# Optimization experiments

Measured on AMD Instinct MI355X. Metric: run time of the kernel, lower is better.

Reference implementation:

```python
import jax, jax.numpy as jnp
import numpy as np

DECAY = 0.99
EPS_VQ = 1e-5
EPS_LN = 1e-5


def setup_inputs() -> dict:
    key = jax.random.key(0)
    ks = jax.random.split(key, 6)
    N, DIN, D, K = 32768, 1024, 512, 1024
    return {
        "x": jax.random.normal(ks[0], (N, DIN), dtype=jnp.float32),
        "enc_w": jax.random.normal(ks[1], (DIN, D), dtype=jnp.float32) * (1.0 / np.sqrt(DIN)),
        "enc_b": jnp.zeros((D,), jnp.float32),
        "ln_g": jnp.ones((D,), jnp.float32),
        "ln_b": jnp.zeros((D,), jnp.float32),
        "dec_w": jax.random.normal(ks[2], (D, DIN), dtype=jnp.float32) * (1.0 / np.sqrt(D)),
        "dec_b": jnp.zeros((DIN,), jnp.float32),
        "embeddings": jax.random.normal(ks[3], (K, D), dtype=jnp.float32),
        "cluster_size": jnp.ones((K,), jnp.float32),
        "ema_embed_sum": jax.random.normal(ks[4], (K, D), dtype=jnp.float32),
    }


def _layernorm(h, g, b):
    mu = jnp.mean(h, axis=-1, keepdims=True)
    var = jnp.var(h, axis=-1, keepdims=True)
    return (h - mu) * jax.lax.rsqrt(var + EPS_LN) * g + b


def reference(x, enc_w, enc_b, ln_g, ln_b, dec_w, dec_b, embeddings, cluster_size, ema_embed_sum):
    K = embeddings.shape[0]
    # encoder: Linear + LayerNorm
    z_e = _layernorm(x @ enc_w + enc_b, ln_g, ln_b)  # [N, D]
    # pairwise squared L2 distances, expanded GEMM form (same argmin as (z-e)^2.sum)
    d = (jnp.sum(z_e * z_e, axis=1, keepdims=True)
         - 2.0 * (z_e @ embeddings.T)
         + jnp.sum(embeddings * embeddings, axis=1)[None, :])  # [N, K]
    indices = jnp.argmin(d, axis=1)  # [N]
    z_q = embeddings[indices]  # gather [N, D]
    # EMA codebook update (training path; buffers, no grad)
    zd = jax.lax.stop_gradient(z_e)
    counts = jax.ops.segment_sum(jnp.ones_like(indices, jnp.float32), indices, num_segments=K)
    embed_sum = jax.ops.segment_sum(zd, indices, num_segments=K)  # one_hot.T @ z
    new_cluster_size = DECAY * cluster_size + (1.0 - DECAY) * counts
    new_ema_embed_sum = DECAY * ema_embed_sum + (1.0 - DECAY) * embed_sum
    n = jnp.sum(new_cluster_size)
    cs = (new_cluster_size + EPS_VQ) / (n + K * EPS_VQ) * n
    new_embeddings = new_ema_embed_sum / cs[:, None]
    # commitment loss + straight-through estimator
    commit_loss = jnp.mean((z_e - jax.lax.stop_gradient(z_q)) ** 2)
    z_q_st = z_e + jax.lax.stop_gradient(z_q - z_e)
    x_recon = z_q_st @ dec_w + dec_b
    return (x_recon, commit_loss, indices, z_e, z_q_st,
            new_embeddings, new_cluster_size, new_ema_embed_sum)
```

## Files before the change

kernel.cpp:

```cpp
#include <hip/hip_runtime.h>

typedef unsigned long long u64;
typedef unsigned int u32;
typedef _Float16 f16;
typedef _Float16 f16x8 __attribute__((ext_vector_type(8)));
typedef float f32x4 __attribute__((ext_vector_type(4)));

#define MFMA16(a, b, c) __builtin_amdgcn_mfma_f32_16x16x32_f16(a, b, c, 0, 0, 0)

#define NROWS 32768
#define DIN   1024
#define DM    512
#define KC    1024
#define SPLIT_SC  1024.0f
#define SPLIT_INV 0.0009765625f
#define CHSZ  32
#define MAXCH 2048
#define MARGIN 0.5f

#define OFF_XR   0ull
#define OFF_CL   33554432ull
#define OFF_IDX  33554433ull
#define OFF_ZE   33587201ull
#define OFF_ZQ   50364417ull
#define OFF_NE   67141633ull
#define OFF_NCS  67665921ull
#define OFF_NEMA 67666945ull

#define WS_ZNORM   2359296ull
#define WS_IDX     2490368ull
#define WS_COUNTS  2621440ull
#define WS_STARTS  2625536ull
#define WS_OFFW    2629632ull
#define WS_ROWLIST 2633728ull
#define WS_CSD     2764800ull
#define WS_ENORM   2769920ull
#define WS2_CAND   (4ull<<20)
#define WS2_WT1    (36ull<<20)
#define WS2_WT2    (37ull<<20)
#define WS2_DT     (38ull<<20)
#define WS2_E1     (39ull<<20)
#define WS3_CHPFX  (41ull<<20)
#define WS3_CHCODE ((41ull<<20) + 8192)
#define WS3_CPART  ((41ull<<20) + 16384)
#define WS3_PART   ((41ull<<20) + 65536)

__device__ inline void gload16(const f16* g, f16* l) {
  __builtin_amdgcn_global_load_lds((const __attribute__((address_space(1))) void*)g,
                                   (__attribute__((address_space(3))) void*)l, 16, 0, 0);
}

__device__ inline f16x8 ldfrag32(const f16* p, int row, int kc) {
  return *(const f16x8*)(p + row * 32 + ((kc ^ ((row >> 1) & 3)) << 3));
}

__device__ inline void stage32(const f16* gbase, int ld, int row0, int k0,
                               f16* lds, int t) {
  int r = t >> 2, c = t & 3;
  int cs = c ^ ((r >> 1) & 3);
  gload16(gbase + (size_t)(row0 + r) * ld + k0 + cs * 8, lds + t * 8);
}

__device__ inline void stageA256(const f16* gbase, int ld, int row0, int k0,
                                 f16* lds, int t) {
#pragma unroll
  for (int h = 0; h < 2; h++) {
    int e = t + h * 512;
    int r = e >> 2, c = e & 3;
    int cs = c ^ ((r >> 1) & 3);
    gload16(gbase + (size_t)(row0 + r) * ld + k0 + cs * 8, lds + e * 8);
  }
}

#define BAR2      { asm volatile("s_waitcnt lgkmcnt(0)" ::: "memory"); \
                    __builtin_amdgcn_s_barrier(); \
                    asm volatile("" ::: "memory"); }

__device__ inline u32 enc_score(float s) {
  u32 kb = __float_as_uint(s);
  return (kb & 0x80000000u) ? ~kb : (kb | 0x80000000u);
}
__device__ inline float dec_score(u32 u) {
  u32 b = (u & 0x80000000u) ? (u & 0x7fffffffu) : ~u;
  return __uint_as_float(b);
}

__global__ __launch_bounds__(256) void k_prep(const float* __restrict__ enc_w,
                                              const float* __restrict__ dec_w,
                                              const float* __restrict__ emb,
                                              f16* __restrict__ wt1,
                                              f16* __restrict__ wt2,
                                              f16* __restrict__ dT,
                                              f16* __restrict__ e1,
                                              float* __restrict__ enorm,
                                              int* __restrict__ counts) {
  __shared__ float tile[32][33];
  int bid = blockIdx.x, t = threadIdx.x;
  if (bid < 1024) {
    const float* W;
    f16 *o1, *o2;
    int K, N, bx, by;
    if (bid < 512) {
      W = enc_w; o1 = wt1; o2 = wt2; K = DIN; N = DM;
      bx = bid & 15; by = bid >> 4;
    } else {
      int b2 = bid - 512;
      W = dec_w; o1 = dT; o2 = nullptr; K = DM; N = DIN;
      bx = b2 & 31; by = b2 >> 5;
    }
    int tx = t & 31, ty = t >> 5;
    int nb = bx * 32, kb = by * 32;
#pragma unroll
    for (int i = 0; i < 32; i += 8)
      tile[ty + i][tx] = W[(size_t)(kb + ty + i) * N + nb + tx];
    __syncthreads();
#pragma unroll
    for (int i = 0; i < 32; i += 8) {
      float v = tile[tx][ty + i];
      f16 h = (f16)v;
      size_t o = (size_t)(nb + ty + i) * K + kb + tx;
      o1[o] = h;
      if (o2) o2[o] = (f16)((v - (float)h) * SPLIT_SC);
    }
  } else if (bid < 1536) {
    int tid = (bid - 1024) * 256 + t;
    for (int i = tid; i < KC * DM; i += 131072) e1[i] = (f16)emb[i];
  } else if (bid < 1792) {
    int k = (bid - 1536) * 4 + (t >> 6), lane = t & 63;
    float s = 0.f;
#pragma unroll
    for (int j = 0; j < 8; j++) {
      float v = emb[(size_t)k * DM + lane + j * 64];
      s = fmaf(v, v, s);
    }
#pragma unroll
    for (int m = 1; m < 64; m <<= 1) s += __shfl_xor(s, m, 64);
    if (lane == 0) enorm[k] = s;
  } else {
    int i = (bid - 1792) * 256 + t;
    if (i < KC) counts[i] = 0;
  }
}

__global__ __launch_bounds__(512) void k_genc4(const float* __restrict__ x,
                                               const f16* __restrict__ wt1,
                                               const f16* __restrict__ wt2,
                                               const float* __restrict__ bias,
                                               float* __restrict__ dst) {
  __shared__ __align__(16) f16 A1[128 * 32], A2[128 * 32];
  __shared__ __align__(16) f16 B1[2][128 * 32], B2[2][128 * 32];
  int t = threadIdx.x, lane = t & 63, wid = t >> 6;
  int wm = wid >> 2, wn = wid & 3;
  int l = blockIdx.x;
  int xcd = l & 7, s = l >> 3, ct = s & 3;
  int p = ((s >> 2) << 3) | xcd;
  int m0 = p * 128, n0 = ct * 128;
  int r = t >> 2, cg = t & 3;
  int cslot = cg ^ ((r >> 1) & 3);
  const float* ax = x + (size_t)(m0 + r) * DIN + cg * 8;
  f32x4 accA[4][2] = {}, accB[4][2] = {};

#define GCONV(v0, v1)                                                       \
  {                                                                         \
    float a_[8] = {v0.x, v0.y, v0.z, v0.w, v1.x, v1.y, v1.z, v1.w};         \
    f16 h1_[8], h2_[8];                                                     \
    _Pragma("unroll") for (int j_ = 0; j_ < 8; j_++) {                      \
      f16 h_ = (f16)a_[j_];                                                 \
      h1_[j_] = h_;                                                         \
      h2_[j_] = (f16)((a_[j_] - (float)h_) * SPLIT_SC);                     \
    }                                                                       \
    *(f16x8*)(A1 + r * 32 + cslot * 8) = *(f16x8*)h1_;                      \
    *(f16x8*)(A2 + r * 32 + cslot * 8) = *(f16x8*)h2_;                      \
  }

#define GCOMP(buf)                                                          \
  {                                                                         \
    int kc_ = lane >> 4;                                                    \
    f16x8 a1f[4], a2f[4], b1f[2], b2f[2];                                   \
    _Pragma("unroll") for (int m_ = 0; m_ < 4; m_++) {                      \
      int row_ = wm * 64 + m_ * 16 + (lane & 15);                           \
      a1f[m_] = ldfrag32(A1, row_, kc_);                                    \
      a2f[m_] = ldfrag32(A2, row_, kc_);                                    \
    }                                                                       \
    _Pragma("unroll") for (int n_ = 0; n_ < 2; n_++) {                      \
      int row_ = wn * 32 + n_ * 16 + (lane & 15);                           \
      b1f[n_] = ldfrag32(B1[buf], row_, kc_);                               \
      b2f[n_] = ldfrag32(B2[buf], row_, kc_);                               \
    }                                                                       \
    _Pragma("unroll") for (int m_ = 0; m_ < 4; m_++)                        \
      _Pragma("unroll") for (int n_ = 0; n_ < 2; n_++) {                    \
        accA[m_][n_] = MFMA16(a1f[m_], b1f[n_], accA[m_][n_]);              \
        accB[m_][n_] = MFMA16(a1f[m_], b2f[n_], accB[m_][n_]);              \
        accB[m_][n_] = MFMA16(a2f[m_], b1f[n_], accB[m_][n_]);              \
      }                                                                     \
  }

  float4 c0 = *(const float4*)(ax);
  float4 c1 = *(const float4*)(ax + 4);
  float4 n0v = *(const float4*)(ax + 32);
  float4 n1v = *(const float4*)(ax + 36);
  stage32(wt1, DIN, n0, 0, B1[0], t);
  stage32(wt2, DIN, n0, 0, B2[0], t);
  asm volatile("s_waitcnt vmcnt(4)" ::: "memory");

  for (int it = 0; it < 32; ++it) {
    GCONV(c0, c1);
    if (it + 1 < 32) {
      stage32(wt1, DIN, n0, (it + 1) * 32, B1[(it + 1) & 1], t);
      stage32(wt2, DIN, n0, (it + 1) * 32, B2[(it + 1) & 1], t);
    }
    float4 f0, f1;
    if (it + 2 < 32) {
      f0 = *(const float4*)(ax + (it + 2) * 32);
      f1 = *(const float4*)(ax + (it + 2) * 32 + 4);
    }
    if (it <= 29) {
      asm volatile("s_waitcnt vmcnt(4) lgkmcnt(0)" ::: "memory");
    } else if (it == 30) {
      asm volatile("s_waitcnt vmcnt(2) lgkmcnt(0)" ::: "memory");
    } else {
      asm volatile("s_waitcnt vmcnt(0) lgkmcnt(0)" ::: "memory");
    }
    __builtin_amdgcn_sched_barrier(0);
    __builtin_amdgcn_s_barrier();
    asm volatile("" ::: "memory");
    GCOMP(it & 1);
    BAR2;
    c0 = n0v; c1 = n1v; n0v = f0; n1v = f1;
  }
#undef GCONV
#undef GCOMP

#pragma unroll
  for (int m = 0; m < 4; m++)
#pragma unroll
    for (int n = 0; n < 2; n++)
#pragma unroll
      for (int j = 0; j < 4; j++) {
        int row = m0 + wm * 64 + m * 16 + (lane >> 4) * 4 + j;
        int col = n0 + wn * 32 + n * 16 + (lane & 15);
        dst[(size_t)row * DM + col] = accA[m][n][j] + SPLIT_INV * accB[m][n][j] + bias[col];
      }
}

__global__ __launch_bounds__(512, 4) void k_dist4(const f16* __restrict__ z1,
                                                  const f16* __restrict__ e1,
                                                  const float* __restrict__ enorm,
                                                  u64* __restrict__ cand) {
  __shared__ __align__(16) f16 A[3][256 * 32];
  __shared__ __align__(16) f16 B[3][128 * 32];
  int t = threadIdx.x, lane = t & 63, wid = t >> 6;
  int wr = wid >> 1, wc = wid & 1;
  int l = blockIdx.x;
  int xcd = l & 7, s = l >> 3, ct = s & 7;
  int p = ((s >> 3) << 3) | xcd;
  int r0 = p * 256, c0 = ct * 128;
  f32x4 acc[4][4] = {};
  int kc = lane >> 4;

  stageA256(z1, DM, r0, 0, A[0], t);
  stage32(e1, DM, c0, 0, B[0], t);

  for (int it = 0; it < 16; ++it) {
    int buf = it % 3;
    if (it < 15) {
      int nb = (it + 1) % 3;
      int k0n = (it + 1) * 32;
      stageA256(z1, DM, r0, k0n, A[nb], t);
      stage32(e1, DM, c0, k0n, B[nb], t);
      asm volatile("s_waitcnt vmcnt(3)" ::: "memory");
    } else {
      asm volatile("s_waitcnt vmcnt(0)" ::: "memory");
    }
    __builtin_amdgcn_sched_barrier(0);
    __builtin_amdgcn_s_barrier();
    asm volatile("" ::: "memory");
    f16x8 af[4], bf[4];
#pragma unroll
    for (int m = 0; m < 4; m++)
      af[m] = ldfrag32(A[buf], wr * 64 + m * 16 + (lane & 15), kc);
#pragma unroll
    for (int n = 0; n < 4; n++)
      bf[n] = ldfrag32(B[buf], wc * 64 + n * 16 + (lane & 15), kc);
#pragma unroll
    for (int m = 0; m < 4; m++)
#pragma unroll
      for (int n = 0; n < 4; n++) acc[m][n] = MFMA16(af[m], bf[n], acc[m][n]);
  }

  __syncthreads();
  u64 (*cand_s)[4] = (u64 (*)[4])(&A[0][0]);
  float en[4];
#pragma unroll
  for (int n = 0; n < 4; n++)
    en[n] = enorm[c0 + wc * 64 + n * 16 + (lane & 15)];
#pragma unroll
  for (int m = 0; m < 4; m++)
#pragma unroll
    for (int j = 0; j < 4; j++) {
      int r_l = wr * 64 + m * 16 + (lane >> 4) * 4 + j;
      u64 lo = ~0ull, hi = ~0ull;
#pragma unroll
      for (int n = 0; n < 4; n++) {
        int col = c0 + wc * 64 + n * 16 + (lane & 15);
        float sc = fmaf(-2.0f, acc[m][n][j], en[n]);
        u64 k = ((u64)enc_score(sc) << 32) | (u32)col;
        if (k < lo) { hi = lo; lo = k; }
        else if (k < hi) { hi = k; }
      }
#pragma unroll
      for (int msk = 1; msk < 16; msk <<= 1) {
        u64 lo2 = __shfl_xor(lo, msk, 64);
        u64 hi2 = __shfl_xor(hi, msk, 64);
        u64 nlo = lo < lo2 ? lo : lo2;
        u64 losr = lo < lo2 ? lo2 : lo;
        u64 nh = hi < hi2 ? hi : hi2;
        hi = losr < nh ? losr : nh;
        lo = nlo;
      }
      if ((lane & 15) == 0) {
        cand_s[r_l][wc * 2] = lo;
        cand_s[r_l][wc * 2 + 1] = hi;
      }
    }
  __syncthreads();
  if (t < 256) {
    u64 b0 = ~0ull, b1 = ~0ull;
#pragma unroll
    for (int i = 0; i < 4; i++) {
      u64 k = cand_s[t][i];
      if (k < b0) { b1 = b0; b0 = k; }
      else if (k < b1) { b1 = k; }
    }
    u64* dst = cand + ((size_t)(r0 + t) * 16 + ct * 2);
    dst[0] = b0;
    dst[1] = b1;
  }
}

__global__ __launch_bounds__(512) void k_edgemm(const f16* __restrict__ e1,
                                                const f16* __restrict__ dT,
                                                const float* __restrict__ bias,
                                                float* __restrict__ ED) {
  __shared__ __align__(16) f16 A[3][128 * 32], B[3][128 * 32];
  int t = threadIdx.x, lane = t & 63, wid = t >> 6;
  int wm = wid >> 2, wn = wid & 3;
  int r0 = (blockIdx.x >> 3) * 128, c0 = (blockIdx.x & 7) * 128;
  f32x4 acc[4][2] = {};
  int kc = lane >> 4;

  stage32(e1, DM, r0, 0, A[0], t);
  stage32(dT, DM, c0, 0, B[0], t);

  for (int it = 0; it < 16; ++it) {
    int buf = it % 3;
    if (it < 15) {
      int nb = (it + 1) % 3;
      int k0n = (it + 1) * 32;
      stage32(e1, DM, r0, k0n, A[nb], t);
      stage32(dT, DM, c0, k0n, B[nb], t);
      asm volatile("s_waitcnt vmcnt(2)" ::: "memory");
    } else {
      asm volatile("s_waitcnt vmcnt(0)" ::: "memory");
    }
    __builtin_amdgcn_sched_barrier(0);
    __builtin_amdgcn_s_barrier();
    asm volatile("" ::: "memory");
    f16x8 af[4], bf[2];
#pragma unroll
    for (int m = 0; m < 4; m++)
      af[m] = ldfrag32(A[buf], wm * 64 + m * 16 + (lane & 15), kc);
#pragma unroll
    for (int n = 0; n < 2; n++)
      bf[n] = ldfrag32(B[buf], wn * 32 + n * 16 + (lane & 15), kc);
#pragma unroll
    for (int m = 0; m < 4; m++)
#pragma unroll
      for (int n = 0; n < 2; n++) acc[m][n] = MFMA16(af[m], bf[n], acc[m][n]);
  }

#pragma unroll
  for (int m = 0; m < 4; m++)
#pragma unroll
    for (int n = 0; n < 2; n++)
#pragma unroll
      for (int j = 0; j < 4; j++) {
        int row = r0 + wm * 64 + m * 16 + (lane >> 4) * 4 + j;
        int col = c0 + wn * 32 + n * 16 + (lane & 15);
        ED[(size_t)row * DIN + col] = acc[m][n][j] + bias[col];
      }
}

__global__ __launch_bounds__(256) void k_gatherx(const int* __restrict__ idxws,
                                                 const float* __restrict__ ED,
                                                 float* __restrict__ xr) {
  int t = threadIdx.x, r0 = blockIdx.x * 16;
  __shared__ int idx_s[16];
  if (t < 16) idx_s[t] = idxws[r0 + t];
  __syncthreads();
  for (int rr = 0; rr < 16; rr++) {
    int R = r0 + rr;
    const float4* src = (const float4*)(ED + (size_t)idx_s[rr] * DIN);
    float4* dst = (float4*)(xr + (size_t)R * DIN);
    dst[t] = src[t];
  }
}

__global__ __launch_bounds__(256) void k_resolve(const u64* __restrict__ cand,
                                                 const float* __restrict__ znorm,
                                                 const float* __restrict__ enorm,
                                                 const float* __restrict__ emb,
                                                 float* __restrict__ out,
                                                 int* __restrict__ idxws,
                                                 int* __restrict__ counts,
                                                 float* __restrict__ cpart) {
  int t = threadIdx.x, bid = blockIdx.x;
  int r0 = bid * 16;
  __shared__ u64 key_s[256];
  __shared__ int idx_s[16];
  __shared__ float commit_s[16];
  __shared__ int flagcnt_s;
  __shared__ int flagrow_s[16];
  key_s[t] = cand[(size_t)r0 * 16 + t];
  if (t == 0) flagcnt_s = 0;
  __syncthreads();

  if (t < 16) {
    u64 best = ~0ull;
#pragma unroll
    for (int i = 0; i < 16; i++) {
      u64 k = key_s[t * 16 + i];
      best = k < best ? k : best;
    }
    float smin = dec_score((u32)(best >> 32));
    float thr = smin + MARGIN;
    int nc = 0;
#pragma unroll
    for (int i = 0; i < 16; i++)
      if (dec_score((u32)(key_s[t * 16 + i] >> 32)) <= thr) nc++;
    idx_s[t] = (int)(u32)(best & 0xffffffffull);
    commit_s[t] = znorm[r0 + t] + smin;
    if (nc > 1) {
      int pz = atomicAdd(&flagcnt_s, 1);
      flagrow_s[pz] = t;
    }
  }
  __syncthreads();

  if (t < 64) {
    int nf = flagcnt_s;
    for (int fi = 0; fi < nf; fi++) {
      int lr = flagrow_s[fi];
      int R = r0 + lr;
      u64 amin = ~0ull;
      for (int i = 0; i < 16; i++) {
        u64 k = key_s[lr * 16 + i];
        amin = k < amin ? k : amin;
      }
      float thr = dec_score((u32)(amin >> 32)) + MARGIN;
      float zn = znorm[R];
      const float* z = out + OFF_ZE + (size_t)R * DM;
      u64 bestk = ~0ull;
      for (int i = 0; i < 16; i++) {
        u64 k = key_s[lr * 16 + i];
        if (dec_score((u32)(k >> 32)) > thr) continue;
        int c = (int)(u32)(k & 0xffffffffull);
        const float* e = emb + (size_t)c * DM;
        float pdot = 0.f;
#pragma unroll
        for (int j = 0; j < 8; j++) pdot = fmaf(z[t + j * 64], e[t + j * 64], pdot);
#pragma unroll
        for (int m = 1; m < 64; m <<= 1) pdot += __shfl_xor(pdot, m, 64);
        float d = fmaf(-2.0f, pdot, zn) + enorm[c];
        u64 pk = ((u64)enc_score(d) << 32) | (u32)c;
        bestk = pk < bestk ? pk : bestk;
      }
      if (t == 0) {
        idx_s[lr] = (int)(u32)(bestk & 0xffffffffull);
        commit_s[lr] = dec_score((u32)(bestk >> 32));
      }
    }
  }
  __syncthreads();

  if (t < 16) {
    int R = r0 + t;
    int idx = idx_s[t];
    out[OFF_IDX + R] = (float)idx;
    idxws[R] = idx;
    atomicAdd(counts + idx, 1);
  }
  __syncthreads();
  for (int rr = 0; rr < 16; rr++) {
    int R = r0 + rr;
    const float* e = emb + (size_t)idx_s[rr] * DM;
    float* zq = out + OFF_ZQ + (size_t)R * DM;
#pragma unroll
    for (int j = 0; j < 2; j++) {
      int c = t + j * 256;
      zq[c] = e[c];
    }
  }
  if (t == 0) {
    float s = 0.f;
#pragma unroll
    for (int i = 0; i < 16; i++) s += commit_s[i];
    cpart[bid] = s;
  }
}

__global__ __launch_bounds__(256) void k_ln3(float* __restrict__ ze,
                                             const float* __restrict__ g,
                                             const float* __restrict__ b,
                                             f16* __restrict__ z1,
                                             float* __restrict__ znorm) {
  int t = threadIdx.x, lane = t & 63, wid = t >> 6;
  int R = blockIdx.x * 4 + wid;
  float* row = ze + (size_t)R * DM;
  float v[8];
  float s = 0.f, sq = 0.f;
#pragma unroll
  for (int j = 0; j < 8; j++) {
    v[j] = row[lane + j * 64];
    s += v[j];
    sq = fmaf(v[j], v[j], sq);
  }
#pragma unroll
  for (int m = 1; m < 64; m <<= 1) {
    s += __shfl_xor(s, m, 64);
    sq += __shfl_xor(sq, m, 64);
  }
  float mu = s * (1.f / DM);
  float var = sq * (1.f / DM) - mu * mu;
  float rs = rsqrtf(var + 1e-5f);
  float zn = 0.f;
#pragma unroll
  for (int j = 0; j < 8; j++) {
    int c = lane + j * 64;
    float o = (v[j] - mu) * rs * g[c] + b[c];
    row[c] = o;
    z1[(size_t)R * DM + c] = (f16)o;
    zn = fmaf(o, o, zn);
  }
#pragma unroll
  for (int m = 1; m < 64; m <<= 1) zn += __shfl_xor(zn, m, 64);
  if (lane == 0) znorm[R] = zn;
}

__global__ __launch_bounds__(1024) void k_scan(const int* __restrict__ counts,
                                               const float* __restrict__ cs_in,
                                               float* __restrict__ out,
                                               int* __restrict__ starts,
                                               int* __restrict__ offw,
                                               float* __restrict__ csd,
                                               const float* __restrict__ cpart,
                                               int* __restrict__ chpfx,
                                               int* __restrict__ chcode) {
  __shared__ float f[1024];
  __shared__ int ib[1024];
  int t = threadIdx.x;
  f[t] = cpart[t] + cpart[t + 1024];
  __syncthreads();
  for (int s = 512; s > 0; s >>= 1) {
    if (t < s) f[t] += f[t + s];
    __syncthreads();
  }
  if (t == 0) out[OFF_CL] = f[0] * (1.f / ((float)NROWS * (float)DM));
  __syncthreads();

  int cnt = counts[t];
  float ncs = 0.99f * cs_in[t] + 0.01f * (float)cnt;
  out[OFF_NCS + t] = ncs;
  f[t] = ncs;
  __syncthreads();
  for (int s = 512; s > 0; s >>= 1) {
    if (t < s) f[t] += f[t + s];
    __syncthreads();
  }
  float n = f[0];
  csd[t] = (ncs + 1e-5f) / (n + (float)KC * 1e-5f) * n;
  ib[t] = cnt;
  __syncthreads();
  for (int s = 1; s < 1024; s <<= 1) {
    int y = (t >= s) ? ib[t - s] : 0;
    __syncthreads();
    ib[t] += y;
    __syncthreads();
  }
  int excl = ib[t] - cnt;
  starts[t] = excl;
  offw[t] = excl;
  int nch = (cnt + CHSZ - 1) / CHSZ;
  __syncthreads();
  ib[t] = nch;
  __syncthreads();
  for (int s = 1; s < 1024; s <<= 1) {
    int y = (t >= s) ? ib[t - s] : 0;
    __syncthreads();
    ib[t] += y;
    __syncthreads();
  }
  int chx = ib[t] - nch;
  chpfx[t] = chx;
  if (t == KC - 1) chpfx[KC] = ib[t];
  for (int j = 0; j < nch; j++) chcode[chx + j] = t;
}

__global__ __launch_bounds__(256) void k_scatter(const int* __restrict__ idxws,
                                                 int* __restrict__ offw,
                                                 int* __restrict__ rowlist) {
  int r = blockIdx.x * 256 + threadIdx.x;
  int idx = idxws[r];
  int pos = atomicAdd(offw + idx, 1);
  rowlist[pos] = r;
}

__global__ __launch_bounds__(128) void k_partsum(const int* __restrict__ chpfx,
                                                 const int* __restrict__ chcode,
                                                 const int* __restrict__ starts,
                                                 const int* __restrict__ counts,
                                                 const int* __restrict__ rowlist,
                                                 const float* __restrict__ out,
                                                 float* __restrict__ part) {
  int c = blockIdx.x, t = threadIdx.x;
  if (c >= chpfx[KC]) return;
  int code = chcode[c];
  int j = c - chpfx[code];
  int ofs = starts[code] + j * CHSZ;
  int len = min(CHSZ, counts[code] - j * CHSZ);
  __shared__ int rl[CHSZ];
  if (t < len) rl[t] = rowlist[ofs + t];
  __syncthreads();
  const float* zeb = out + OFF_ZE;
  float a0 = 0.f, a1 = 0.f, a2 = 0.f, a3 = 0.f;
  for (int i = 0; i < len; i++) {
    const float* z = zeb + (size_t)rl[i] * DM;
    a0 += z[t];
    a1 += z[t + 128];
    a2 += z[t + 256];
    a3 += z[t + 384];
  }
  float* pp = part + (size_t)c * DM;
  pp[t] = a0;
  pp[t + 128] = a1;
  pp[t + 256] = a2;
  pp[t + 384] = a3;
}

__global__ __launch_bounds__(128) void k_codesum2(const int* __restrict__ chpfx,
                                                  const float* __restrict__ part,
                                                  const float* __restrict__ ema_in,
                                                  const float* __restrict__ csd,
                                                  float* __restrict__ out) {
  int k = blockIdx.x, t = threadIdx.x;
  int base = chpfx[k], nch = chpfx[k + 1] - base;
  float a0 = 0.f, a1 = 0.f, a2 = 0.f, a3 = 0.f;
  for (int i = 0; i < nch; i++) {
    const float* pp = part + (size_t)(base + i) * DM;
    a0 += pp[t];
    a1 += pp[t + 128];
    a2 += pp[t + 256];
    a3 += pp[t + 384];
  }
  float cs = csd[k];
  float sum[4] = {a0, a1, a2, a3};
#pragma unroll
  for (int j = 0; j < 4; j++) {
    int c = t + j * 128;
    float e = 0.99f * ema_in[(size_t)k * DM + c] + 0.01f * sum[j];
    out[OFF_NEMA + (size_t)k * DM + c] = e;
    out[OFF_NE + (size_t)k * DM + c] = e / cs;
  }
}

extern "C" void kernel_launch(void* const* d_in, const int* in_sizes, int n_in,
                              void* d_out, int out_size, void* d_ws, size_t ws_size,
                              hipStream_t stream) {
  (void)in_sizes; (void)n_in; (void)out_size; (void)ws_size;
  const float* x = (const float*)d_in[0];
  const float* enc_w = (const float*)d_in[1];
  const float* enc_b = (const float*)d_in[2];
  const float* ln_g = (const float*)d_in[3];
  const float* ln_b = (const float*)d_in[4];
  const float* dec_w = (const float*)d_in[5];
  const float* dec_b = (const float*)d_in[6];
  const float* emb = (const float*)d_in[7];
  const float* cs_in = (const float*)d_in[8];
  const float* ema_in = (const float*)d_in[9];
  float* out = (float*)d_out;
  char* ws = (char*)d_ws;
  float* znorm = (float*)(ws + WS_ZNORM);
  int* idxws = (int*)(ws + WS_IDX);
  int* counts = (int*)(ws + WS_COUNTS);
  int* starts = (int*)(ws + WS_STARTS);
  int* offw = (int*)(ws + WS_OFFW);
  int* rowlist = (int*)(ws + WS_ROWLIST);
  float* csd = (float*)(ws + WS_CSD);
  float* enorm = (float*)(ws + WS_ENORM);
  u64* cand = (u64*)(ws + WS2_CAND);
  float* ED = (float*)(ws + WS2_CAND);
  f16* wt1 = (f16*)(ws + WS2_WT1);
  f16* wt2 = (f16*)(ws + WS2_WT2);
  f16* dT = (f16*)(ws + WS2_DT);
  f16* e1 = (f16*)(ws + WS2_E1);
  int* chpfx = (int*)(ws + WS3_CHPFX);
  int* chcode = (int*)(ws + WS3_CHCODE);
  float* cpart = (float*)(ws + WS3_CPART);
  float* part = (float*)(ws + WS3_PART);
  f16* z1 = (f16*)out;

  k_prep<<<dim3(1796), dim3(256), 0, stream>>>(enc_w, dec_w, emb, wt1, wt2, dT,
                                               e1, enorm, counts);
  k_genc4<<<dim3(1024), dim3(512), 0, stream>>>(x, wt1, wt2, enc_b, out + OFF_ZE);
  k_ln3<<<dim3(8192), dim3(256), 0, stream>>>(out + OFF_ZE, ln_g, ln_b, z1, znorm);
  k_dist4<<<dim3(1024), dim3(512), 0, stream>>>(z1, e1, enorm, cand);
  k_resolve<<<dim3(2048), dim3(256), 0, stream>>>(cand, znorm, enorm, emb, out,
                                                  idxws, counts, cpart);
  k_edgemm<<<dim3(64), dim3(512), 0, stream>>>(e1, dT, dec_b, ED);
  k_scan<<<dim3(1), dim3(1024), 0, stream>>>(counts, cs_in, out, starts, offw, csd,
                                             cpart, chpfx, chcode);
  k_scatter<<<dim3(NROWS / 256), dim3(256), 0, stream>>>(idxws, offw, rowlist);
  k_partsum<<<dim3(MAXCH), dim3(128), 0, stream>>>(chpfx, chcode, starts, counts,
                                                   rowlist, out, part);
  k_codesum2<<<dim3(KC), dim3(128), 0, stream>>>(chpfx, part, ema_in, csd, out);
  k_gatherx<<<dim3(2048), dim3(256), 0, stream>>>(idxws, ED, out + OFF_XR);
}
```

Before: 336.7 us.

## Use single fp16 encoder GEMM and recompute ambiguous rows in fp32

Replaces the split-precision (hi/lo fp16, three MFMAs per tile) encoder GEMM with a plain fp16 GEMM over a pre-converted fp16 copy of x, using a larger 256x128 tile with a triple-buffered LDS pipeline. Rows whose nearest-code decision falls within a margin are collected into a global flag list, and a new kernel recomputes their encoder output and LayerNorm in fp32 to re-pick the code and patch indices, counts and z_q. This cuts MFMA work and the on-the-fly conversion, at the cost of an extra x conversion pass and an fp32 fix-up pass. z_e, the commit loss and the EMA sums still come from the lower-precision GEMM, so output accuracy may drop.

```diff
diff --git a/kernel.cpp b/kernel.cpp
--- a/kernel.cpp
+++ b/kernel.cpp
@@ -4,6 +4,7 @@
 typedef unsigned int u32;
 typedef _Float16 f16;
 typedef _Float16 f16x8 __attribute__((ext_vector_type(8)));
+typedef _Float16 f16x4 __attribute__((ext_vector_type(4)));
 typedef float f32x4 __attribute__((ext_vector_type(4)));
 
 #define MFMA16(a, b, c) __builtin_amdgcn_mfma_f32_16x16x32_f16(a, b, c, 0, 0, 0)
@@ -13,10 +14,10 @@
 #define DM    512
 #define KC    1024
 #define SPLIT_SC  1024.0f
-#define SPLIT_INV 0.0009765625f
 #define CHSZ  32
 #define MAXCH 2048
 #define MARGIN 0.5f
+#define ZB    8
 
 #define OFF_XR   0ull
 #define OFF_CL   33554432ull
@@ -27,6 +28,7 @@
 #define OFF_NCS  67665921ull
 #define OFF_NEMA 67666945ull
 
+#define WS_FLAG    2097152ull
 #define WS_ZNORM   2359296ull
 #define WS_IDX     2490368ull
 #define WS_COUNTS  2621440ull
@@ -37,13 +39,14 @@
 #define WS_ENORM   2769920ull
 #define WS2_CAND   (4ull<<20)
 #define WS2_WT1    (36ull<<20)
-#define WS2_WT2    (37ull<<20)
 #define WS2_DT     (38ull<<20)
 #define WS2_E1     (39ull<<20)
 #define WS3_CHPFX  (41ull<<20)
 #define WS3_CHCODE ((41ull<<20) + 8192)
 #define WS3_CPART  ((41ull<<20) + 16384)
+#define WS3_NFLAG  ((41ull<<20) + 32768)
 #define WS3_PART   ((41ull<<20) + 65536)
+
 
 __device__ inline void gload16(const f16* g, f16* l) {
   __builtin_amdgcn_global_load_lds((const __attribute__((address_space(1))) void*)g,
@@ -72,10 +75,6 @@
   }
 }
 
-#define BAR2      { asm volatile("s_waitcnt lgkmcnt(0)" ::: "memory"); \
-                    __builtin_amdgcn_s_barrier(); \
-                    asm volatile("" ::: "memory"); }
-
 __device__ inline u32 enc_score(float s) {
   u32 kb = __float_as_uint(s);
   return (kb & 0x80000000u) ? ~kb : (kb | 0x80000000u);
@@ -88,24 +87,26 @@
 __global__ __launch_bounds__(256) void k_prep(const float* __restrict__ enc_w,
                                               const float* __restrict__ dec_w,
                                               const float* __restrict__ emb,
+                                              const float* __restrict__ x,
                                               f16* __restrict__ wt1,
-                                              f16* __restrict__ wt2,
                                               f16* __restrict__ dT,
                                               f16* __restrict__ e1,
+                                              f16* __restrict__ x16,
                                               float* __restrict__ enorm,
-                                              int* __restrict__ counts) {
+                                              int* __restrict__ counts,
+                                              int* __restrict__ nflag) {
   __shared__ float tile[32][33];
   int bid = blockIdx.x, t = threadIdx.x;
   if (bid < 1024) {
     const float* W;
-    f16 *o1, *o2;
+    f16* o1;
     int K, N, bx, by;
     if (bid < 512) {
-      W = enc_w; o1 = wt1; o2 = wt2; K = DIN; N = DM;
+      W = enc_w; o1 = wt1; K = DIN; N = DM;
       bx = bid & 15; by = bid >> 4;
     } else {
       int b2 = bid - 512;
-      W = dec_w; o1 = dT; o2 = nullptr; K = DM; N = DIN;
+      W = dec_w; o1 = dT; K = DM; N = DIN;
       bx = b2 & 31; by = b2 >> 5;
     }
     int tx = t & 31, ty = t >> 5;
@@ -115,13 +116,8 @@
       tile[ty + i][tx] = W[(size_t)(kb + ty + i) * N + nb + tx];
     __syncthreads();
 #pragma unroll
-    for (int i = 0; i < 32; i += 8) {
-      float v = tile[tx][ty + i];
-      f16 h = (f16)v;
-      size_t o = (size_t)(nb + ty + i) * K + kb + tx;
-      o1[o] = h;
-      if (o2) o2[o] = (f16)((v - (float)h) * SPLIT_SC);
-    }
+    for (int i = 0; i < 32; i += 8)
+      o1[(size_t)(nb + ty + i) * K + kb + tx] = (f16)tile[tx][ty + i];
   } else if (bid < 1536) {
     int tid = (bid - 1024) * 256 + t;
     for (int i = tid; i < KC * DM; i += 131072) e1[i] = (f16)emb[i];
@@ -136,110 +132,74 @@
 #pragma unroll
     for (int m = 1; m < 64; m <<= 1) s += __shfl_xor(s, m, 64);
     if (lane == 0) enorm[k] = s;
-  } else {
+  } else if (bid < 1796) {
     int i = (bid - 1792) * 256 + t;
     if (i < KC) counts[i] = 0;
-  }
-}
-
-__global__ __launch_bounds__(512) void k_genc4(const float* __restrict__ x,
-                                               const f16* __restrict__ wt1,
-                                               const f16* __restrict__ wt2,
-                                               const float* __restrict__ bias,
-                                               float* __restrict__ dst) {
-  __shared__ __align__(16) f16 A1[128 * 32], A2[128 * 32];
-  __shared__ __align__(16) f16 B1[2][128 * 32], B2[2][128 * 32];
+    if (bid == 1792 && t == 0) nflag[0] = 0;
+  } else {
+    size_t base = (size_t)(bid - 1796) * 16384;
+    for (int i = t; i < 4096; i += 256) {
+      float4 v = *(const float4*)(x + base + (size_t)i * 4);
+      f16 h4[4] = {(f16)v.x, (f16)v.y, (f16)v.z, (f16)v.w};
+      *(f16x4*)(x16 + base + (size_t)i * 4) = *(f16x4*)h4;
+    }
+  }
+}
+
+__global__ __launch_bounds__(512, 4) void k_genc1p(const f16* __restrict__ x16,
+                                                   const f16* __restrict__ wt1,
+                                                   const float* __restrict__ bias,
+                                                   float* __restrict__ dst) {
+  __shared__ __align__(16) f16 A[3][256 * 32];
+  __shared__ __align__(16) f16 B[3][128 * 32];
   int t = threadIdx.x, lane = t & 63, wid = t >> 6;
-  int wm = wid >> 2, wn = wid & 3;
+  int wr = wid >> 1, wc = wid & 1;
   int l = blockIdx.x;
   int xcd = l & 7, s = l >> 3, ct = s & 3;
   int p = ((s >> 2) << 3) | xcd;
-  int m0 = p * 128, n0 = ct * 128;
-  int r = t >> 2, cg = t & 3;
-  int cslot = cg ^ ((r >> 1) & 3);
-  const float* ax = x + (size_t)(m0 + r) * DIN + cg * 8;
-  f32x4 accA[4][2] = {}, accB[4][2] = {};
-
-#define GCONV(v0, v1)                                                       \
-  {                                                                         \
-    float a_[8] = {v0.x, v0.y, v0.z, v0.w, v1.x, v1.y, v1.z, v1.w};         \
-    f16 h1_[8], h2_[8];                                                     \
-    _Pragma("unroll") for (int j_ = 0; j_ < 8; j_++) {                      \
-      f16 h_ = (f16)a_[j_];                                                 \
-      h1_[j_] = h_;                                                         \
-      h2_[j_] = (f16)((a_[j_] - (float)h_) * SPLIT_SC);                     \
-    }                                                                       \
-    *(f16x8*)(A1 + r * 32 + cslot * 8) = *(f16x8*)h1_;                      \
-    *(f16x8*)(A2 + r * 32 + cslot * 8) = *(f16x8*)h2_;                      \
-  }
-
-#define GCOMP(buf)                                                          \
-  {                                                                         \
-    int kc_ = lane >> 4;                                                    \
-    f16x8 a1f[4], a2f[4], b1f[2], b2f[2];                                   \
-    _Pragma("unroll") for (int m_ = 0; m_ < 4; m_++) {                      \
-      int row_ = wm * 64 + m_ * 16 + (lane & 15);                           \
-      a1f[m_] = ldfrag32(A1, row_, kc_);                                    \
-      a2f[m_] = ldfrag32(A2, row_, kc_);                                    \
-    }                                                                       \
-    _Pragma("unroll") for (int n_ = 0; n_ < 2; n_++) {                      \
-      int row_ = wn * 32 + n_ * 16 + (lane & 15);                           \
-      b1f[n_] = ldfrag32(B1[buf], row_, kc_);                               \
-      b2f[n_] = ldfrag32(B2[buf], row_, kc_);                               \
-    }                                                                       \
-    _Pragma("unroll") for (int m_ = 0; m_ < 4; m_++)                        \
-      _Pragma("unroll") for (int n_ = 0; n_ < 2; n_++) {                    \
-        accA[m_][n_] = MFMA16(a1f[m_], b1f[n_], accA[m_][n_]);              \
-        accB[m_][n_] = MFMA16(a1f[m_], b2f[n_], accB[m_][n_]);              \
-        accB[m_][n_] = MFMA16(a2f[m_], b1f[n_], accB[m_][n_]);              \
-      }                                                                     \
-  }
-
-  float4 c0 = *(const float4*)(ax);
-  float4 c1 = *(const float4*)(ax + 4);
-  float4 n0v = *(const float4*)(ax + 32);
-  float4 n1v = *(const float4*)(ax + 36);
-  stage32(wt1, DIN, n0, 0, B1[0], t);
-  stage32(wt2, DIN, n0, 0, B2[0], t);
-  asm volatile("s_waitcnt vmcnt(4)" ::: "memory");
+  int r0 = p * 256, c0 = ct * 128;
+  f32x4 acc[4][4] = {};
+  int kc = lane >> 4;
+
+  stageA256(x16, DIN, r0, 0, A[0], t);
+  stage32(wt1, DIN, c0, 0, B[0], t);
 
   for (int it = 0; it < 32; ++it) {
-    GCONV(c0, c1);
-    if (it + 1 < 32) {
-      stage32(wt1, DIN, n0, (it + 1) * 32, B1[(it + 1) & 1], t);
-      stage32(wt2, DIN, n0, (it + 1) * 32, B2[(it + 1) & 1], t);
-    }
-    float4 f0, f1;
-    if (it + 2 < 32) {
-      f0 = *(const float4*)(ax + (it + 2) * 32);
-      f1 = *(const float4*)(ax + (it + 2) * 32 + 4);
-    }
-    if (it <= 29) {
-      asm volatile("s_waitcnt vmcnt(4) lgkmcnt(0)" ::: "memory");
-    } else if (it == 30) {
-      asm volatile("s_waitcnt vmcnt(2) lgkmcnt(0)" ::: "memory");
+    int buf = it % 3;
+    if (it < 31) {
+      int nb = (it + 1) % 3;
+      int k0n = (it + 1) * 32;
+      stageA256(x16, DIN, r0, k0n, A[nb], t);
+      stage32(wt1, DIN, c0, k0n, B[nb], t);
+      asm volatile("s_waitcnt vmcnt(3)" ::: "memory");
     } else {
-      asm volatile("s_waitcnt vmcnt(0) lgkmcnt(0)" ::: "memory");
+      asm volatile("s_waitcnt vmcnt(0)" ::: "memory");
     }
     __builtin_amdgcn_sched_barrier(0);
     __builtin_amdgcn_s_barrier();
     asm volatile("" ::: "memory");
-    GCOMP(it & 1);
-    BAR2;
-    c0 = n0v; c1 = n1v; n0v = f0; n1v = f1;
-  }
-#undef GCONV
-#undef GCOMP
+    f16x8 af[4], bf[4];
+#pragma unroll
+    for (int m = 0; m < 4; m++)
+      af[m] = ldfrag32(A[buf], wr * 64 + m * 16 + (lane & 15), kc);
+#pragma unroll
+    for (int n = 0; n < 4; n++)
+      bf[n] = ldfrag32(B[buf], wc * 64 + n * 16 + (lane & 15), kc);
+#pragma unroll
+    for (int m = 0; m < 4; m++)
+#pragma unroll
+      for (int n = 0; n < 4; n++) acc[m][n] = MFMA16(af[m], bf[n], acc[m][n]);
+  }
 
 #pragma unroll
   for (int m = 0; m < 4; m++)
 #pragma unroll
-    for (int n = 0; n < 2; n++)
+    for (int n = 0; n < 4; n++)
 #pragma unroll
       for (int j = 0; j < 4; j++) {
-        int row = m0 + wm * 64 + m * 16 + (lane >> 4) * 4 + j;
-        int col = n0 + wn * 32 + n * 16 + (lane & 15);
-        dst[(size_t)row * DM + col] = accA[m][n][j] + SPLIT_INV * accB[m][n][j] + bias[col];
+        int row = r0 + wr * 64 + m * 16 + (lane >> 4) * 4 + j;
+        int col = c0 + wc * 64 + n * 16 + (lane & 15);
+        dst[(size_t)row * DM + col] = acc[m][n][j] + bias[col];
       }
 }
 
@@ -338,6 +298,182 @@
   }
 }
 
+__global__ __launch_bounds__(256) void k_resolve(const u64* __restrict__ cand,
+                                                 const float* __restrict__ znorm,
+                                                 const float* __restrict__ emb,
+                                                 float* __restrict__ out,
+                                                 int* __restrict__ idxws,
+                                                 int* __restrict__ counts,
+                                                 float* __restrict__ cpart,
+                                                 int* __restrict__ nflag,
+                                                 int* __restrict__ flaglist) {
+  int t = threadIdx.x, bid = blockIdx.x;
+  int r0 = bid * 16;
+  __shared__ u64 key_s[256];
+  __shared__ int idx_s[16];
+  __shared__ float commit_s[16];
+  key_s[t] = cand[(size_t)r0 * 16 + t];
+  __syncthreads();
+
+  if (t < 16) {
+    int R = r0 + t;
+    u64 best = ~0ull;
+#pragma unroll
+    for (int i = 0; i < 16; i++) {
+      u64 k = key_s[t * 16 + i];
+      best = k < best ? k : best;
+    }
+    float smin = dec_score((u32)(best >> 32));
+    float thr = smin + MARGIN;
+    int nc = 0;
+#pragma unroll
+    for (int i = 0; i < 16; i++)
+      if (dec_score((u32)(key_s[t * 16 + i] >> 32)) <= thr) nc++;
+    int idx = (int)(u32)(best & 0xffffffffull);
+    idx_s[t] = idx;
+    commit_s[t] = znorm[R] + smin;
+    if (nc > 1) {
+      int pz = atomicAdd(nflag, 1);
+      flaglist[pz] = R;
+    }
+    out[OFF_IDX + R] = (float)idx;
+    idxws[R] = idx;
+    atomicAdd(counts + idx, 1);
+  }
+  __syncthreads();
+  for (int rr = 0; rr < 16; rr++) {
+    int R = r0 + rr;
+    const float* e = emb + (size_t)idx_s[rr] * DM;
+    float* zq = out + OFF_ZQ + (size_t)R * DM;
+#pragma unroll
+    for (int j = 0; j < 2; j++) {
+      int c = t + j * 256;
+      zq[c] = e[c];
+    }
+  }
+  if (t == 0) {
+    float s = 0.f;
+#pragma unroll
+    for (int i = 0; i < 16; i++) s += commit_s[i];
+    cpart[bid] = s;
+  }
+}
+
+__global__ __launch_bounds__(512) void k_zfix(const int* __restrict__ nflag,
+                                              const int* __restrict__ flaglist,
+                                              const float* __restrict__ x,
+                                              const float* __restrict__ enc_w,
+                                              const float* __restrict__ enc_b,
+                                              const float* __restrict__ g,
+                                              const float* __restrict__ bb,
+                                              const u64* __restrict__ cand,
+                                              const float* __restrict__ emb,
+                                              const float* __restrict__ enorm,
+                                              float* __restrict__ out,
+                                              int* __restrict__ idxws,
+                                              int* __restrict__ counts) {
+  __shared__ float xs[ZB][1024];
+  __shared__ float zs[ZB][512];
+  __shared__ float red[ZB][8], red2[ZB][8];
+  __shared__ int rows_s[ZB];
+  int nf = nflag[0];
+  int t = threadIdx.x, lane = t & 63, wid = t >> 6;
+  for (int b = blockIdx.x; b * ZB < nf; b += 128) {
+    int base = b * ZB;
+    int cnt = min(ZB, nf - base);
+    if (t < ZB) rows_s[t] = flaglist[base + min(t, cnt - 1)];
+    __syncthreads();
+    for (int i = t; i < cnt * 256; i += 512) {
+      int r8 = i >> 8, c4 = (i & 255) << 2;
+      *(float4*)&xs[r8][c4] = *(const float4*)(x + (size_t)rows_s[r8] * DIN + c4);
+    }
+    __syncthreads();
+    float acc[ZB];
+#pragma unroll
+    for (int r = 0; r < ZB; r++) acc[r] = 0.f;
+    for (int k = 0; k < 1024; k += 4) {
+      float w0 = enc_w[(size_t)k * DM + t];
+      float w1 = enc_w[(size_t)(k + 1) * DM + t];
+      float w2 = enc_w[(size_t)(k + 2) * DM + t];
+      float w3 = enc_w[(size_t)(k + 3) * DM + t];
+#pragma unroll
+      for (int r = 0; r < ZB; r++) {
+        float4 xv = *(const float4*)&xs[r][k];
+        acc[r] = fmaf(xv.x, w0, acc[r]);
+        acc[r] = fmaf(xv.y, w1, acc[r]);
+        acc[r] = fmaf(xv.z, w2, acc[r]);
+        acc[r] = fmaf(xv.w, w3, acc[r]);
+      }
+    }
+    float bsum = enc_b[t];
+#pragma unroll
+    for (int r = 0; r < ZB; r++) {
+      acc[r] += bsum;
+      float s = acc[r], sq = acc[r] * acc[r];
+#pragma unroll
+      for (int m = 1; m < 64; m <<= 1) {
+        s += __shfl_xor(s, m, 64);
+        sq += __shfl_xor(sq, m, 64);
+      }
+      if (lane == 0) { red[r][wid] = s; red2[r][wid] = sq; }
+    }
+    __syncthreads();
+    float gg = g[t], bv = bb[t];
+#pragma unroll
+    for (int r = 0; r < ZB; r++) {
+      float s = 0.f, sq = 0.f;
+#pragma unroll
+      for (int w8 = 0; w8 < 8; w8++) { s += red[r][w8]; sq += red2[r][w8]; }
+      float mu = s * (1.f / DM);
+      float var = sq * (1.f / DM) - mu * mu;
+      float rs = rsqrtf(var + 1e-5f);
+      zs[r][t] = (acc[r] - mu) * rs * gg + bv;
+    }
+    __syncthreads();
+    if (wid < cnt) {
+      int R = rows_s[wid];
+      float zreg[8];
+      float zn = 0.f;
+#pragma unroll
+      for (int j = 0; j < 8; j++) {
+        zreg[j] = zs[wid][lane + j * 64];
+        zn = fmaf(zreg[j], zreg[j], zn);
+      }
+#pragma unroll
+      for (int m = 1; m < 64; m <<= 1) zn += __shfl_xor(zn, m, 64);
+      u64 bestk = ~0ull;
+      for (int i = 0; i < 16; i++) {
+        u64 kk = cand[(size_t)R * 16 + i];
+        int c = (int)(u32)(kk & 0xffffffffull);
+        const float* e = emb + (size_t)c * DM;
+        float dot = 0.f;
+#pragma unroll
+        for (int j = 0; j < 8; j++) dot = fmaf(zreg[j], e[lane + j * 64], dot);
+#pragma unroll
+        for (int m = 1; m < 64; m <<= 1) dot += __shfl_xor(dot, m, 64);
+        float d = fmaf(-2.f, dot, zn) + enorm[c];
+        u64 pk = ((u64)enc_score(d) << 32) | (u32)c;
+        bestk = pk < bestk ? pk : bestk;
+      }
+      int newidx = (int)(u32)(bestk & 0xffffffffull);
+      int oldidx = idxws[R];
+      if (newidx != oldidx) {
+        if (lane == 0) {
+          idxws[R] = newidx;
+          out[OFF_IDX + R] = (float)newidx;
+          atomicSub(counts + oldidx, 1);
+          atomicAdd(counts + newidx, 1);
+        }
+        const float* e = emb + (size_t)newidx * DM;
+        float* zq = out + OFF_ZQ + (size_t)R * DM;
+#pragma unroll
+        for (int j = 0; j < 8; j++) zq[lane + j * 64] = e[lane + j * 64];
+      }
+    }
+    __syncthreads();
+  }
+}
+
 __global__ __launch_bounds__(512) void k_edgemm(const f16* __restrict__ e1,
                                                 const f16* __restrict__ dT,
                                                 const float* __restrict__ bias,
@@ -403,109 +539,6 @@
     const float4* src = (const float4*)(ED + (size_t)idx_s[rr] * DIN);
     float4* dst = (float4*)(xr + (size_t)R * DIN);
     dst[t] = src[t];
-  }
-}
-
-__global__ __launch_bounds__(256) void k_resolve(const u64* __restrict__ cand,
-                                                 const float* __restrict__ znorm,
-                                                 const float* __restrict__ enorm,
-                                                 const float* __restrict__ emb,
-                                                 float* __restrict__ out,
-                                                 int* __restrict__ idxws,
-                                                 int* __restrict__ counts,
-                                                 float* __restrict__ cpart) {
-  int t = threadIdx.x, bid = blockIdx.x;
-  int r0 = bid * 16;
-  __shared__ u64 key_s[256];
-  __shared__ int idx_s[16];
-  __shared__ float commit_s[16];
-  __shared__ int flagcnt_s;
-  __shared__ int flagrow_s[16];
-  key_s[t] = cand[(size_t)r0 * 16 + t];
-  if (t == 0) flagcnt_s = 0;
-  __syncthreads();
-
-  if (t < 16) {
-    u64 best = ~0ull;
-#pragma unroll
-    for (int i = 0; i < 16; i++) {
-      u64 k = key_s[t * 16 + i];
-      best = k < best ? k : best;
-    }
-    float smin = dec_score((u32)(best >> 32));
-    float thr = smin + MARGIN;
-    int nc = 0;
-#pragma unroll
-    for (int i = 0; i < 16; i++)
-      if (dec_score((u32)(key_s[t * 16 + i] >> 32)) <= thr) nc++;
-    idx_s[t] = (int)(u32)(best & 0xffffffffull);
-    commit_s[t] = znorm[r0 + t] + smin;
-    if (nc > 1) {
-      int pz = atomicAdd(&flagcnt_s, 1);
-      flagrow_s[pz] = t;
-    }
-  }
-  __syncthreads();
-
-  if (t < 64) {
-    int nf = flagcnt_s;
-    for (int fi = 0; fi < nf; fi++) {
-      int lr = flagrow_s[fi];
-      int R = r0 + lr;
-      u64 amin = ~0ull;
-      for (int i = 0; i < 16; i++) {
-        u64 k = key_s[lr * 16 + i];
-        amin = k < amin ? k : amin;
-      }
-      float thr = dec_score((u32)(amin >> 32)) + MARGIN;
-      float zn = znorm[R];
-      const float* z = out + OFF_ZE + (size_t)R * DM;
-      u64 bestk = ~0ull;
-      for (int i = 0; i < 16; i++) {
-        u64 k = key_s[lr * 16 + i];
-        if (dec_score((u32)(k >> 32)) > thr) continue;
-        int c = (int)(u32)(k & 0xffffffffull);
-        const float* e = emb + (size_t)c * DM;
-        float pdot = 0.f;
-#pragma unroll
-        for (int j = 0; j < 8; j++) pdot = fmaf(z[t + j * 64], e[t + j * 64], pdot);
-#pragma unroll
-        for (int m = 1; m < 64; m <<= 1) pdot += __shfl_xor(pdot, m, 64);
-        float d = fmaf(-2.0f, pdot, zn) + enorm[c];
-        u64 pk = ((u64)enc_score(d) << 32) | (u32)c;
-        bestk = pk < bestk ? pk : bestk;
-      }
-      if (t == 0) {
-        idx_s[lr] = (int)(u32)(bestk & 0xffffffffull);
-        commit_s[lr] = dec_score((u32)(bestk >> 32));
-      }
-    }
-  }
-  __syncthreads();
-
-  if (t < 16) {
-    int R = r0 + t;
-    int idx = idx_s[t];
-    out[OFF_IDX + R] = (float)idx;
-    idxws[R] = idx;
-    atomicAdd(counts + idx, 1);
-  }
-  __syncthreads();
-  for (int rr = 0; rr < 16; rr++) {
-    int R = r0 + rr;
-    const float* e = emb + (size_t)idx_s[rr] * DM;
-    float* zq = out + OFF_ZQ + (size_t)R * DM;
-#pragma unroll
-    for (int j = 0; j < 2; j++) {
-      int c = t + j * 256;
-      zq[c] = e[c];
-    }
-  }
-  if (t == 0) {
-    float s = 0.f;
-#pragma unroll
-    for (int i = 0; i < 16; i++) s += commit_s[i];
-    cpart[bid] = s;
   }
 }
 
@@ -689,6 +722,7 @@
   const float* ema_in = (const float*)d_in[9];
   float* out = (float*)d_out;
   char* ws = (char*)d_ws;
+  int* flaglist = (int*)(ws + WS_FLAG);
   float* znorm = (float*)(ws + WS_ZNORM);
   int* idxws = (int*)(ws + WS_IDX);
   int* counts = (int*)(ws + WS_COUNTS);
@@ -700,22 +734,26 @@
   u64* cand = (u64*)(ws + WS2_CAND);
   float* ED = (float*)(ws + WS2_CAND);
   f16* wt1 = (f16*)(ws + WS2_WT1);
-  f16* wt2 = (f16*)(ws + WS2_WT2);
   f16* dT = (f16*)(ws + WS2_DT);
   f16* e1 = (f16*)(ws + WS2_E1);
   int* chpfx = (int*)(ws + WS3_CHPFX);
   int* chcode = (int*)(ws + WS3_CHCODE);
   float* cpart = (float*)(ws + WS3_CPART);
+  int* nflag = (int*)(ws + WS3_NFLAG);
   float* part = (float*)(ws + WS3_PART);
   f16* z1 = (f16*)out;
-
-  k_prep<<<dim3(1796), dim3(256), 0, stream>>>(enc_w, dec_w, emb, wt1, wt2, dT,
-                                               e1, enorm, counts);
-  k_genc4<<<dim3(1024), dim3(512), 0, stream>>>(x, wt1, wt2, enc_b, out + OFF_ZE);
+  f16* x16 = (f16*)((char*)out + (32ull << 20));
+
+  k_prep<<<dim3(3844), dim3(256), 0, stream>>>(enc_w, dec_w, emb, x, wt1, dT,
+                                               e1, x16, enorm, counts, nflag);
+  k_genc1p<<<dim3(512), dim3(512), 0, stream>>>(x16, wt1, enc_b, out + OFF_ZE);
   k_ln3<<<dim3(8192), dim3(256), 0, stream>>>(out + OFF_ZE, ln_g, ln_b, z1, znorm);
   k_dist4<<<dim3(1024), dim3(512), 0, stream>>>(z1, e1, enorm, cand);
-  k_resolve<<<dim3(2048), dim3(256), 0, stream>>>(cand, znorm, enorm, emb, out,
-                                                  idxws, counts, cpart);
+  k_resolve<<<dim3(2048), dim3(256), 0, stream>>>(cand, znorm, emb, out, idxws,
+                                                  counts, cpart, nflag, flaglist);
+  k_zfix<<<dim3(128), dim3(512), 0, stream>>>(nflag, flaglist, x, enc_w, enc_b,
+                                              ln_g, ln_b, cand, emb, enorm, out,
+                                              idxws, counts);
   k_edgemm<<<dim3(64), dim3(512), 0, stream>>>(e1, dT, dec_b, ED);
   k_scan<<<dim3(1), dim3(1024), 0, stream>>>(counts, cs_in, out, starts, offw, csd,
                                              cpart, chpfx, chcode);
```

Measured after the change: 429.3 us. +27.5%, slower.

## Double-buffer A tiles in encoder GEMM to drop one barrier per step

Applied to the files above, without the earlier changes.

The encoder GEMM now double-buffers the converted fp16 A tiles (hi/lo split) in LDS. The conversion of the next x slice moves to after the MFMA compute of the current one, so each iteration needs one workgroup barrier instead of two. It also adds a 4-waves-per-EU occupancy hint to launch_bounds. LDS use grows to 64 KB per block, which may limit how many blocks fit per CU, and the vmcnt wait counts were rewritten by hand to match the new load order.

```diff
diff --git a/kernel.cpp b/kernel.cpp
--- a/kernel.cpp
+++ b/kernel.cpp
@@ -71,10 +71,6 @@
     gload16(gbase + (size_t)(row0 + r) * ld + k0 + cs * 8, lds + e * 8);
   }
 }
-
-#define BAR2      { asm volatile("s_waitcnt lgkmcnt(0)" ::: "memory"); \
-                    __builtin_amdgcn_s_barrier(); \
-                    asm volatile("" ::: "memory"); }
 
 __device__ inline u32 enc_score(float s) {
   u32 kb = __float_as_uint(s);
@@ -142,12 +138,12 @@
   }
 }
 
-__global__ __launch_bounds__(512) void k_genc4(const float* __restrict__ x,
-                                               const f16* __restrict__ wt1,
-                                               const f16* __restrict__ wt2,
-                                               const float* __restrict__ bias,
-                                               float* __restrict__ dst) {
-  __shared__ __align__(16) f16 A1[128 * 32], A2[128 * 32];
+__global__ __launch_bounds__(512, 4) void k_genc6(const float* __restrict__ x,
+                                                  const f16* __restrict__ wt1,
+                                                  const f16* __restrict__ wt2,
+                                                  const float* __restrict__ bias,
+                                                  float* __restrict__ dst) {
+  __shared__ __align__(16) f16 A1[2][128 * 32], A2[2][128 * 32];
   __shared__ __align__(16) f16 B1[2][128 * 32], B2[2][128 * 32];
   int t = threadIdx.x, lane = t & 63, wid = t >> 6;
   int wm = wid >> 2, wn = wid & 3;
@@ -160,7 +156,7 @@
   const float* ax = x + (size_t)(m0 + r) * DIN + cg * 8;
   f32x4 accA[4][2] = {}, accB[4][2] = {};
 
-#define GCONV(v0, v1)                                                       \
+#define GCONV(v0, v1, buf)                                                  \
   {                                                                         \
     float a_[8] = {v0.x, v0.y, v0.z, v0.w, v1.x, v1.y, v1.z, v1.w};         \
     f16 h1_[8], h2_[8];                                                     \
@@ -169,8 +165,8 @@
       h1_[j_] = h_;                                                         \
       h2_[j_] = (f16)((a_[j_] - (float)h_) * SPLIT_SC);                     \
     }                                                                       \
-    *(f16x8*)(A1 + r * 32 + cslot * 8) = *(f16x8*)h1_;                      \
-    *(f16x8*)(A2 + r * 32 + cslot * 8) = *(f16x8*)h2_;                      \
+    *(f16x8*)(A1[buf] + r * 32 + cslot * 8) = *(f16x8*)h1_;                 \
+    *(f16x8*)(A2[buf] + r * 32 + cslot * 8) = *(f16x8*)h2_;                 \
   }
 
 #define GCOMP(buf)                                                          \
@@ -179,8 +175,8 @@
     f16x8 a1f[4], a2f[4], b1f[2], b2f[2];                                   \
     _Pragma("unroll") for (int m_ = 0; m_ < 4; m_++) {                      \
       int row_ = wm * 64 + m_ * 16 + (lane & 15);                           \
-      a1f[m_] = ldfrag32(A1, row_, kc_);                                    \
-      a2f[m_] = ldfrag32(A2, row_, kc_);                                    \
+      a1f[m_] = ldfrag32(A1[buf], row_, kc_);                               \
+      a2f[m_] = ldfrag32(A2[buf], row_, kc_);                               \
     }                                                                       \
     _Pragma("unroll") for (int n_ = 0; n_ < 2; n_++) {                      \
       int row_ = wn * 32 + n_ * 16 + (lane & 15);                           \
@@ -197,14 +193,18 @@
 
   float4 c0 = *(const float4*)(ax);
   float4 c1 = *(const float4*)(ax + 4);
+  stage32(wt1, DIN, n0, 0, B1[0], t);
+  stage32(wt2, DIN, n0, 0, B2[0], t);
   float4 n0v = *(const float4*)(ax + 32);
   float4 n1v = *(const float4*)(ax + 36);
-  stage32(wt1, DIN, n0, 0, B1[0], t);
-  stage32(wt2, DIN, n0, 0, B2[0], t);
   asm volatile("s_waitcnt vmcnt(4)" ::: "memory");
+  GCONV(c0, c1, 0);
+  asm volatile("s_waitcnt vmcnt(2) lgkmcnt(0)" ::: "memory");
+  __builtin_amdgcn_sched_barrier(0);
+  __builtin_amdgcn_s_barrier();
+  asm volatile("" ::: "memory");
 
   for (int it = 0; it < 32; ++it) {
-    GCONV(c0, c1);
     if (it + 1 < 32) {
       stage32(wt1, DIN, n0, (it + 1) * 32, B1[(it + 1) & 1], t);
       stage32(wt2, DIN, n0, (it + 1) * 32, B2[(it + 1) & 1], t);
@@ -214,19 +214,24 @@
       f0 = *(const float4*)(ax + (it + 2) * 32);
       f1 = *(const float4*)(ax + (it + 2) * 32 + 4);
     }
-    if (it <= 29) {
-      asm volatile("s_waitcnt vmcnt(4) lgkmcnt(0)" ::: "memory");
-    } else if (it == 30) {
-      asm volatile("s_waitcnt vmcnt(2) lgkmcnt(0)" ::: "memory");
-    } else {
-      asm volatile("s_waitcnt vmcnt(0) lgkmcnt(0)" ::: "memory");
-    }
-    __builtin_amdgcn_sched_barrier(0);
-    __builtin_amdgcn_s_barrier();
-    asm volatile("" ::: "memory");
     GCOMP(it & 1);
-    BAR2;
-    c0 = n0v; c1 = n1v; n0v = f0; n1v = f1;
+    if (it + 1 < 32) {
+      if (it <= 29) {
+        asm volatile("s_waitcnt vmcnt(4)" ::: "memory");
+      } else {
+        asm volatile("s_waitcnt vmcnt(2)" ::: "memory");
+      }
+      GCONV(n0v, n1v, (it + 1) & 1);
+      if (it <= 29) {
+        asm volatile("s_waitcnt vmcnt(2) lgkmcnt(0)" ::: "memory");
+      } else {
+        asm volatile("s_waitcnt vmcnt(0) lgkmcnt(0)" ::: "memory");
+      }
+      __builtin_amdgcn_sched_barrier(0);
+      __builtin_amdgcn_s_barrier();
+      asm volatile("" ::: "memory");
+    }
+    n0v = f0; n1v = f1;
   }
 #undef GCONV
 #undef GCOMP
@@ -711,7 +716,7 @@
 
   k_prep<<<dim3(1796), dim3(256), 0, stream>>>(enc_w, dec_w, emb, wt1, wt2, dT,
                                                e1, enorm, counts);
-  k_genc4<<<dim3(1024), dim3(512), 0, stream>>>(x, wt1, wt2, enc_b, out + OFF_ZE);
+  k_genc6<<<dim3(1024), dim3(512), 0, stream>>>(x, wt1, wt2, enc_b, out + OFF_ZE);
   k_ln3<<<dim3(8192), dim3(256), 0, stream>>>(out + OFF_ZE, ln_g, ln_b, z1, znorm);
   k_dist4<<<dim3(1024), dim3(512), 0, stream>>>(z1, e1, enorm, cand);
   k_resolve<<<dim3(2048), dim3(256), 0, stream>>>(cand, znorm, enorm, emb, out,
```

Result: no change. 331.7 us (-1.5%).
